# Optimization experiments

Hardware: AMD Instinct MI355X
Metric: run time of the kernel (lower is better)

## Reference

```python
import jax, jax.numpy as jnp
import numpy as np

NEG_INF = -10000.0  # module uses inf = 10000.0, not true infinity
B, S, N_TAGS, N_LABELS, N_PATTERNS = 256, 1024, 64, 32, 4


def setup_inputs() -> dict:
    key = jax.random.key(0)
    ks = jax.random.split(key, 8)
    label_emissions = jax.random.normal(ks[0], (B, S, N_LABELS), jnp.float32)
    pattern_emissions = jax.random.normal(ks[1], (B, S, N_PATTERNS), jnp.float32)
    y = jax.random.randint(ks[2], (B, S), 0, N_TAGS)
    label_transitions = 0.1 * jax.random.normal(ks[3], (N_LABELS, N_LABELS), jnp.float32)
    tag2label = jax.random.randint(ks[4], (N_TAGS,), 0, N_LABELS)
    tag_patterns = jax.random.bernoulli(ks[5], 0.25, (N_TAGS, N_PATTERNS)).astype(jnp.float32)
    allowed = jax.random.bernoulli(ks[6], 0.5, (N_TAGS, N_TAGS))
    transition_constraints = jnp.where(allowed, 0.0, NEG_INF).astype(jnp.float32)
    start_mask = jax.random.bernoulli(ks[7], 0.3, (N_TAGS,))
    start_mask = start_mask.at[0].set(True)  # ensure at least one start tag
    return dict(label_emissions=label_emissions,
                pattern_emissions=pattern_emissions,
                y=y,
                label_transitions=label_transitions,
                tag2label=tag2label,
                tag_patterns=tag_patterns,
                transition_constraints=transition_constraints,
                start_mask=start_mask)


def _log_p(label_emissions, pattern_emissions, label_transitions,
           tag_patterns, transition_constraints, y, tag2label, start_mask):
    # per-tag potentials x: [B, S, T]
    x = label_emissions[:, :, tag2label] + pattern_emissions @ tag_patterns.T
    # _transitions(): label_transitions.view(-1)[indices] + constraints == outer gather
    transitions = label_transitions[tag2label[:, None], tag2label[None, :]] + transition_constraints  # [T, T]

    # ----- _logZ (forward algorithm, enforce_boundaries=True) -----
    init = jnp.where(start_mask[None, :], x[:, 0, :], NEG_INF)  # [B, T]

    def step(logits, xi):
        # logmmexp(logits, transitions) + xi
        new = jax.nn.logsumexp(logits[:, :, None] + transitions[None, :, :], axis=1) + xi
        return new, None

    xs = jnp.moveaxis(x[:, 1:, :], 1, 0)  # [S-1, B, T]
    final, _ = jax.lax.scan(step, init, xs)
    logZ = jax.nn.logsumexp(final, axis=1)  # [B]

    # ----- _score -----
    emission = jnp.take_along_axis(x, y[:, :, None], axis=2)[:, :, 0].sum(axis=1)  # [B]
    trans = transitions[y[:, :-1], y[:, 1:]].sum(axis=1)  # [B]
    return emission + trans - logZ


def reference(label_emissions, pattern_emissions, y, label_transitions,
              tag2label, tag_patterns, transition_constraints, start_mask):
    return _log_p(label_emissions, pattern_emissions, label_transitions,
                  tag_patterns, transition_constraints, y, tag2label, start_mask)
```

## Files before the change

### kernel.cpp

```cpp
#include <hip/hip_runtime.h>

#define LOG2E 1.4426950408889634f
#define LN2   0.6931471805599453f
#define PSC   8.0f

typedef __attribute__((ext_vector_type(8))) short bf16x8;
typedef __attribute__((ext_vector_type(4))) float f32x4;
typedef __attribute__((ext_vector_type(4))) unsigned u32x4;

__device__ __forceinline__ unsigned pk_bf16(float lo, float hi){
  unsigned r;
  asm("v_cvt_pk_bf16_f32 %0, %1, %2" : "=v"(r) : "v"(lo), "v"(hi));
  return r;
}
__device__ __forceinline__ unsigned short bf16_rne(float x){
  unsigned u = __float_as_uint(x);
  return (unsigned short)((u + 0x7FFFu + ((u>>16)&1u)) >> 16);
}

__device__ __forceinline__ float wave_sum64(float v){
#define DADD(ctrl) { int _t = __builtin_amdgcn_update_dpp(0, __float_as_int(v), ctrl, 0xF, 0xF, false); \
                     v = v + __int_as_float(_t); }
  DADD(0x111) DADD(0x112) DADD(0x114) DADD(0x118) DADD(0x142) DADD(0x143)
#undef DADD
  return __int_as_float(__builtin_amdgcn_readlane(__float_as_int(v), 63));
}
__device__ __forceinline__ float wave_max64(float v){
#define DMAX(ctrl) { int _t = __builtin_amdgcn_update_dpp(__float_as_int(v), __float_as_int(v), ctrl, 0xF, 0xF, false); \
                     v = fmaxf(v, __int_as_float(_t)); }
  DMAX(0x111) DMAX(0x112) DMAX(0x114) DMAX(0x118) DMAX(0x142) DMAX(0x143)
#undef DMAX
  return __int_as_float(__builtin_amdgcn_readlane(__float_as_int(v), 63));
}
__device__ __forceinline__ f32x4 vmax4(f32x4 a, f32x4 b){
  f32x4 r; r.x=fmaxf(a.x,b.x); r.y=fmaxf(a.y,b.y); r.z=fmaxf(a.z,b.z); r.w=fmaxf(a.w,b.w); return r;
}

__global__ void __launch_bounds__(512, 1)
patcrf_fwd(const float* __restrict__ le, const float* __restrict__ pe,
           const int* __restrict__ y, const float* __restrict__ lt,
           const int* __restrict__ t2l, const float* __restrict__ tp,
           const float* __restrict__ tc, const unsigned int* __restrict__ smask,
           float* __restrict__ out)
{
  const int b = blockIdx.x;
  const int tid = threadIdx.x;
  const int wv = tid >> 6;
  const int lane = tid & 63;
  const int bb = lane & 15, jj = lane >> 4;

  __shared__ __align__(16) char smem[86016];
  float* trans_lds = (float*)smem;
  int*   y_lds     = (int*)(smem + 16384);
  float* E_lds     = (float*)(smem + 20480);
  unsigned short* P_lds = (unsigned short*)smem;
  __shared__ __align__(16) float tp_lds[256];
  __shared__ __align__(16) float pf[64];
  __shared__ int   t2l_lds[64];
  __shared__ float scpart[8];
  __shared__ float L2arr[8];

  if (tid < 64){
    t2l_lds[tid] = t2l[tid];
    *(f32x4*)(tp_lds + tid*4) = *(const f32x4*)(tp + tid*4);
  }
  const int* yb = y + b*1024;
  y_lds[tid] = yb[tid];
  y_lds[tid+512] = yb[tid+512];
  __syncthreads();
  #pragma unroll
  for (int k=0;k<8;k++){
    int idx = k*512 + tid;
    trans_lds[idx] = lt[t2l_lds[idx>>6]*32 + t2l_lds[idx&63]] + tc[idx];
  }
  __syncthreads();

  const float* leb = le + (size_t)b*1024*32;
  const float* peb = pe + (size_t)b*1024*4;
  const int   myl  = t2l_lds[lane];
  const f32x4 mytp = *(const f32x4*)(tp_lds + lane*4);

  {
    int s0 = tid*2;
    int y0 = y_lds[s0], y1 = y_lds[s0+1];
    f32x4 pA = *(const f32x4*)(peb + (size_t)s0*4);
    f32x4 pB = *(const f32x4*)(peb + (size_t)(s0+1)*4);
    f32x4 tA = *(const f32x4*)(tp_lds + y0*4);
    f32x4 tB = *(const f32x4*)(tp_lds + y1*4);
    float s = leb[(size_t)s0*32 + t2l_lds[y0]]
            + pA.x*tA.x + pA.y*tA.y + pA.z*tA.z + pA.w*tA.w
            + leb[(size_t)(s0+1)*32 + t2l_lds[y1]]
            + pB.x*tB.x + pB.y*tB.y + pB.z*tB.z + pB.w*tB.w;
    s += trans_lds[y0*64 + y1];
    if (s0+2 < 1024) s += trans_lds[y1*64 + y_lds[s0+2]];
    float sw = wave_sum64(s);
    if (lane==0) scpart[wv] = sw;
  }

#define CSTEP(ACC, EPTR) do { \
    f32x4 ev[4]; \
    _Pragma("unroll") \
    for (int m_=0;m_<4;m_++) ev[m_] = *(const f32x4*)((EPTR) + 16*m_ + 4*jj); \
    u32x4 Bf[2][4]; \
    _Pragma("unroll") \
    for (int n_=0;n_<4;n_++){ \
      _Pragma("unroll") \
      for (int h_=0;h_<2;h_++){ \
        Bf[h_][n_] = (u32x4){ \
          pk_bf16(ACC[2*h_][n_].x,   ACC[2*h_][n_].y), \
          pk_bf16(ACC[2*h_][n_].z,   ACC[2*h_][n_].w), \
          pk_bf16(ACC[2*h_+1][n_].x, ACC[2*h_+1][n_].y), \
          pk_bf16(ACC[2*h_+1][n_].z, ACC[2*h_+1][n_].w) }; \
      } \
    } \
    _Pragma("unroll") \
    for (int m_=0;m_<4;m_++){ \
      _Pragma("unroll") \
      for (int n_=0;n_<4;n_++){ \
        f32x4 d_ = __builtin_amdgcn_mfma_f32_16x16x32_bf16( \
                     __builtin_bit_cast(bf16x8, Af[m_][0]), \
                     __builtin_bit_cast(bf16x8, Bf[0][n_]), zf, 0,0,0); \
        d_ = __builtin_amdgcn_mfma_f32_16x16x32_bf16( \
                     __builtin_bit_cast(bf16x8, Af[m_][1]), \
                     __builtin_bit_cast(bf16x8, Bf[1][n_]), d_, 0,0,0); \
        ACC[m_][n_] = d_ * ev[m_]; \
      } \
    } \
  } while(0)

#define RENORM(ACC, L2V) do { \
    f32x4 m4_ = ACC[0][0]; \
    _Pragma("unroll") \
    for (int m_=0;m_<4;m_++){ \
      _Pragma("unroll") \
      for (int n_=0;n_<4;n_++) m4_ = vmax4(m4_, ACC[m_][n_]); \
    } \
    float mx_ = fmaxf(fmaxf(m4_.x,m4_.y), fmaxf(m4_.z,m4_.w)); \
    mx_ = wave_max64(mx_); \
    if (mx_ > 0.f){ \
      int Ex_ = (int)(__float_as_uint(mx_)>>23) - 127; \
      if (Ex_ != 0){ \
        float scl_ = __uint_as_float((unsigned)(127 - Ex_) << 23); \
        _Pragma("unroll") \
        for (int m_=0;m_<4;m_++){ \
          _Pragma("unroll") \
          for (int n_=0;n_<4;n_++) ACC[m_][n_] = ACC[m_][n_]*scl_; \
        } \
        (L2V) += (float)Ex_; \
      } \
    } \
  } while(0)

  if (wv < 4){
    const int c = wv;
    u32x4 Af[4][2];
    #pragma unroll
    for (int m=0;m<4;m++){
      #pragma unroll
      for (int h=0;h<2;h++){
        unsigned uu[4];
        #pragma unroll
        for (int q=0;q<4;q++){
          int c0 = 2*q, c1 = 2*q+1;
          int sg0 = 32*h + ((c0>>2)<<4) + 4*jj + (c0&3);
          int sg1 = 32*h + ((c1>>2)<<4) + 4*jj + (c1&3);
          float w0 = __builtin_amdgcn_exp2f(trans_lds[sg0*64 + 16*m + bb]*LOG2E);
          float w1 = __builtin_amdgcn_exp2f(trans_lds[sg1*64 + 16*m + bb]*LOG2E);
          uu[q] = pk_bf16(w0, w1);
        }
        Af[m][h] = (u32x4){uu[0],uu[1],uu[2],uu[3]};
      }
    }
    f32x4 accA[4][4], accB[4][4];
    #pragma unroll
    for (int m=0;m<4;m++){
      #pragma unroll
      for (int n=0;n<4;n++){
        f32x4 z;
        z.x = (m==n && bb==4*jj+0) ? 1.f : 0.f;
        z.y = (m==n && bb==4*jj+1) ? 1.f : 0.f;
        z.z = (m==n && bb==4*jj+2) ? 1.f : 0.f;
        z.w = (m==n && bb==4*jj+3) ? 1.f : 0.f;
        accA[m][n] = z; accB[m][n] = z;
      }
    }
    float L2A = 0.f, L2B = 0.f;
    const f32x4 zf = {0.f,0.f,0.f,0.f};

    __syncthreads();

    for (int ep=0; ep<8; ++ep){
      const float* EbA = E_lds + (c*4 + (ep&1)*2 + 0)*1024;
      const float* EbB = E_lds + (c*4 + (ep&1)*2 + 1)*1024;
      #pragma unroll 2
      for (int s=0;s<16;s++){
        if (!(c==0 && ep==0 && s==0)) CSTEP(accA, EbA + s*64);
        CSTEP(accB, EbB + s*64);
      }
      RENORM(accA, L2A);
      RENORM(accB, L2B);
      __syncthreads();
    }

    {
      unsigned short* PcA = P_lds + (2*c  )*4352;
      unsigned short* PcB = P_lds + (2*c+1)*4352;
      #pragma unroll
      for (int m=0;m<4;m++){
        #pragma unroll
        for (int n=0;n<4;n++){
          PcA[(16*m+4*jj+0)*68 + 16*n + bb] = bf16_rne(accA[m][n].x);
          PcA[(16*m+4*jj+1)*68 + 16*n + bb] = bf16_rne(accA[m][n].y);
          PcA[(16*m+4*jj+2)*68 + 16*n + bb] = bf16_rne(accA[m][n].z);
          PcA[(16*m+4*jj+3)*68 + 16*n + bb] = bf16_rne(accA[m][n].w);
          PcB[(16*m+4*jj+0)*68 + 16*n + bb] = bf16_rne(accB[m][n].x);
          PcB[(16*m+4*jj+1)*68 + 16*n + bb] = bf16_rne(accB[m][n].y);
          PcB[(16*m+4*jj+2)*68 + 16*n + bb] = bf16_rne(accB[m][n].z);
          PcB[(16*m+4*jj+3)*68 + 16*n + bb] = bf16_rne(accB[m][n].w);
        }
      }
      if (lane==0){ L2arr[2*c] = L2A; L2arr[2*c+1] = L2B; }
    }
  } else {
    const int c = wv - 4;
    const int base = 256*c;
    float leA[32]; f32x4 peA[32];
    #pragma unroll
    for (int k=0;k<32;k++){
      int t = base + 128*(k>>4) + (k&15);
      float l0 = leb[(size_t)t*32 + myl];
      f32x4 p0 = *(const f32x4*)(peb + (size_t)t*4);
      float x2 = (l0 + p0.x*mytp.x + p0.y*mytp.y + p0.z*mytp.z + p0.w*mytp.w)*LOG2E - PSC;
      E_lds[(c*4 + (k>>4))*1024 + (k&15)*64 + lane] = __builtin_amdgcn_exp2f(x2);
    }
    #pragma unroll
    for (int k=0;k<32;k++){
      int t = base + 128*(k>>4) + 16 + (k&15);
      leA[k] = leb[(size_t)t*32 + myl];
      peA[k] = *(const f32x4*)(peb + (size_t)t*4);
    }
    __syncthreads();

    for (int ep=0; ep<8; ++ep){
      if (ep < 7){
        int buf = (ep+1)&1;
        #pragma unroll
        for (int k=0;k<32;k++){
          float x2 = (leA[k] + peA[k].x*mytp.x + peA[k].y*mytp.y
                             + peA[k].z*mytp.z + peA[k].w*mytp.w)*LOG2E - PSC;
          E_lds[(c*4 + buf*2 + (k>>4))*1024 + (k&15)*64 + lane] = __builtin_amdgcn_exp2f(x2);
        }
        if (ep < 6){
          #pragma unroll
          for (int k=0;k<32;k++){
            int t = base + 128*(k>>4) + 16*(ep+2) + (k&15);
            leA[k] = leb[(size_t)t*32 + myl];
            peA[k] = *(const f32x4*)(peb + (size_t)t*4);
          }
        }
      }
      __syncthreads();
    }
  }

  __syncthreads();

  if (wv == 0){
    bool all01 = true, allf = true;
    #pragma unroll
    for (int k=0;k<16;k++){
      unsigned v = smask[k];
      all01 = all01 && (v <= 1u);
      allf  = allf  && (v == 0u || v == 0x3F800000u);
    }
    int startv;
    if (all01)      startv = ((const int*)smask)[lane];
    else if (allf)  startv = (((const unsigned*)smask)[lane] != 0u) ? 1 : 0;
    else            startv = ((const unsigned char*)smask)[lane];

    f32x4 pe0 = *(const f32x4*)peb;
    float x0 = leb[myl] + pe0.x*mytp.x + pe0.y*mytp.y + pe0.z*mytp.z + pe0.w*mytp.w;
    float v = startv ? __builtin_amdgcn_exp2f(x0*LOG2E - PSC) : 0.f;
    float L2p = 0.f;

    #pragma unroll 1
    for (int cc=0; cc<8; ++cc){
      pf[lane] = v;
      __builtin_amdgcn_wave_barrier();
      asm volatile("" ::: "memory");
      const unsigned short* Pr = P_lds + cc*4352 + lane*68;
      float q = 0.f;
      #pragma unroll
      for (int k=0;k<16;k++){
        uint2 u = *(const uint2*)(Pr + 4*k);
        f32x4 vv = *(const f32x4*)(pf + 4*k);
        q = fmaf(__uint_as_float(u.x << 16),          vv.x, q);
        q = fmaf(__uint_as_float(u.x & 0xFFFF0000u),  vv.y, q);
        q = fmaf(__uint_as_float(u.y << 16),          vv.z, q);
        q = fmaf(__uint_as_float(u.y & 0xFFFF0000u),  vv.w, q);
      }
      __builtin_amdgcn_wave_barrier();
      asm volatile("" ::: "memory");
      float S = wave_sum64(q);
      L2p += __builtin_amdgcn_logf(S);
      v = q * __builtin_amdgcn_rcpf(S);
    }
    if (lane == 0){
      float sct = ((scpart[0]+scpart[1])+(scpart[2]+scpart[3]))
                + ((scpart[4]+scpart[5])+(scpart[6]+scpart[7]));
      float l2t = ((L2arr[0]+L2arr[1])+(L2arr[2]+L2arr[3]))
                + ((L2arr[4]+L2arr[5])+(L2arr[6]+L2arr[7]));
      float logZ = LN2 * (l2t + L2p + PSC*1024.0f);
      out[b] = sct - logZ;
    }
  }
#undef CSTEP
#undef RENORM
}

extern "C" void kernel_launch(void* const* d_in, const int* in_sizes, int n_in,
                              void* d_out, int out_size, void* d_ws, size_t ws_size,
                              hipStream_t stream)
{
  patcrf_fwd<<<256, 512, 0, stream>>>(
    (const float*)d_in[0],
    (const float*)d_in[1],
    (const int*)d_in[2],
    (const float*)d_in[3],
    (const int*)d_in[4],
    (const float*)d_in[5],
    (const float*)d_in[6],
    (const unsigned int*)d_in[7],
    (float*)d_out);
}
```

Baseline: 119.3 us.

## Make every wave compute its own chunk and emissions instead of producer/consumer split

Replaces the 4 producer + 4 consumer wave split with 8 symmetric waves. Each wave computes exp emissions for its own 128-step chunk into a private double buffer and runs the MFMA chunk product on one accumulator set instead of two interleaved chains. This removes the dedicated producer waves and doubles the number of MFMA-issuing waves, at the cost of each wave serialising its global loads and exps with its own matmul steps. It also adds a guard against a non-positive normaliser in the final combine.

```diff
diff --git a/kernel.cpp b/kernel.cpp
--- a/kernel.cpp
+++ b/kernel.cpp
@@ -151,118 +151,91 @@
     } \
   } while(0)
 
-  if (wv < 4){
-    const int c = wv;
-    u32x4 Af[4][2];
+  const int c = wv;
+  const int base = 128*c;
+  float* Ew = E_lds + wv*2048;
+
+  u32x4 Af[4][2];
+  #pragma unroll
+  for (int m=0;m<4;m++){
     #pragma unroll
-    for (int m=0;m<4;m++){
+    for (int h=0;h<2;h++){
+      unsigned uu[4];
       #pragma unroll
-      for (int h=0;h<2;h++){
-        unsigned uu[4];
-        #pragma unroll
-        for (int q=0;q<4;q++){
-          int c0 = 2*q, c1 = 2*q+1;
-          int sg0 = 32*h + ((c0>>2)<<4) + 4*jj + (c0&3);
-          int sg1 = 32*h + ((c1>>2)<<4) + 4*jj + (c1&3);
-          float w0 = __builtin_amdgcn_exp2f(trans_lds[sg0*64 + 16*m + bb]*LOG2E);
-          float w1 = __builtin_amdgcn_exp2f(trans_lds[sg1*64 + 16*m + bb]*LOG2E);
-          uu[q] = pk_bf16(w0, w1);
-        }
-        Af[m][h] = (u32x4){uu[0],uu[1],uu[2],uu[3]};
+      for (int q=0;q<4;q++){
+        int c0 = 2*q, c1 = 2*q+1;
+        int sg0 = 32*h + ((c0>>2)<<4) + 4*jj + (c0&3);
+        int sg1 = 32*h + ((c1>>2)<<4) + 4*jj + (c1&3);
+        float w0 = __builtin_amdgcn_exp2f(trans_lds[sg0*64 + 16*m + bb]*LOG2E);
+        float w1 = __builtin_amdgcn_exp2f(trans_lds[sg1*64 + 16*m + bb]*LOG2E);
+        uu[q] = pk_bf16(w0, w1);
       }
-    }
-    f32x4 accA[4][4], accB[4][4];
+      Af[m][h] = (u32x4){uu[0],uu[1],uu[2],uu[3]};
+    }
+  }
+  f32x4 acc[4][4];
+  #pragma unroll
+  for (int m=0;m<4;m++){
+    #pragma unroll
+    for (int n=0;n<4;n++){
+      f32x4 z;
+      z.x = (m==n && bb==4*jj+0) ? 1.f : 0.f;
+      z.y = (m==n && bb==4*jj+1) ? 1.f : 0.f;
+      z.z = (m==n && bb==4*jj+2) ? 1.f : 0.f;
+      z.w = (m==n && bb==4*jj+3) ? 1.f : 0.f;
+      acc[m][n] = z;
+    }
+  }
+  float L2c = 0.f;
+  const f32x4 zf = {0.f,0.f,0.f,0.f};
+
+  #pragma unroll
+  for (int s=0;s<16;s++){
+    int t = base + s;
+    float l0 = leb[(size_t)t*32 + myl];
+    f32x4 p0 = *(const f32x4*)(peb + (size_t)t*4);
+    Ew[s*64 + lane] = __builtin_amdgcn_exp2f(
+      (l0 + p0.x*mytp.x + p0.y*mytp.y + p0.z*mytp.z + p0.w*mytp.w)*LOG2E - PSC);
+  }
+  __syncthreads();
+
+  for (int ep=0; ep<8; ++ep){
+    if (ep < 7){
+      float* Eh = Ew + ((ep+1)&1)*1024;
+      #pragma unroll
+      for (int s=0;s<16;s++){
+        int t = base + 16*(ep+1) + s;
+        float l0 = leb[(size_t)t*32 + myl];
+        f32x4 p0 = *(const f32x4*)(peb + (size_t)t*4);
+        Eh[s*64 + lane] = __builtin_amdgcn_exp2f(
+          (l0 + p0.x*mytp.x + p0.y*mytp.y + p0.z*mytp.z + p0.w*mytp.w)*LOG2E - PSC);
+      }
+    }
+    __syncthreads();
+    const float* Eb = Ew + (ep&1)*1024;
+    #pragma unroll 2
+    for (int s=0;s<16;s++){
+      if (!(c==0 && ep==0 && s==0)) CSTEP(acc, Eb + s*64);
+    }
+    RENORM(acc, L2c);
+  }
+
+  __syncthreads();
+
+  {
+    unsigned short* Pc = P_lds + c*4352;
     #pragma unroll
     for (int m=0;m<4;m++){
       #pragma unroll
       for (int n=0;n<4;n++){
-        f32x4 z;
-        z.x = (m==n && bb==4*jj+0) ? 1.f : 0.f;
-        z.y = (m==n && bb==4*jj+1) ? 1.f : 0.f;
-        z.z = (m==n && bb==4*jj+2) ? 1.f : 0.f;
-        z.w = (m==n && bb==4*jj+3) ? 1.f : 0.f;
-        accA[m][n] = z; accB[m][n] = z;
+        Pc[(16*m+4*jj+0)*68 + 16*n + bb] = bf16_rne(acc[m][n].x);
+        Pc[(16*m+4*jj+1)*68 + 16*n + bb] = bf16_rne(acc[m][n].y);
+        Pc[(16*m+4*jj+2)*68 + 16*n + bb] = bf16_rne(acc[m][n].z);
+        Pc[(16*m+4*jj+3)*68 + 16*n + bb] = bf16_rne(acc[m][n].w);
       }
     }
-    float L2A = 0.f, L2B = 0.f;
-    const f32x4 zf = {0.f,0.f,0.f,0.f};
-
-    __syncthreads();
-
-    for (int ep=0; ep<8; ++ep){
-      const float* EbA = E_lds + (c*4 + (ep&1)*2 + 0)*1024;
-      const float* EbB = E_lds + (c*4 + (ep&1)*2 + 1)*1024;
-      #pragma unroll 2
-      for (int s=0;s<16;s++){
-        if (!(c==0 && ep==0 && s==0)) CSTEP(accA, EbA + s*64);
-        CSTEP(accB, EbB + s*64);
-      }
-      RENORM(accA, L2A);
-      RENORM(accB, L2B);
-      __syncthreads();
-    }
-
-    {
-      unsigned short* PcA = P_lds + (2*c  )*4352;
-      unsigned short* PcB = P_lds + (2*c+1)*4352;
-      #pragma unroll
-      for (int m=0;m<4;m++){
-        #pragma unroll
-        for (int n=0;n<4;n++){
-          PcA[(16*m+4*jj+0)*68 + 16*n + bb] = bf16_rne(accA[m][n].x);
-          PcA[(16*m+4*jj+1)*68 + 16*n + bb] = bf16_rne(accA[m][n].y);
-          PcA[(16*m+4*jj+2)*68 + 16*n + bb] = bf16_rne(accA[m][n].z);
-          PcA[(16*m+4*jj+3)*68 + 16*n + bb] = bf16_rne(accA[m][n].w);
-          PcB[(16*m+4*jj+0)*68 + 16*n + bb] = bf16_rne(accB[m][n].x);
-          PcB[(16*m+4*jj+1)*68 + 16*n + bb] = bf16_rne(accB[m][n].y);
-          PcB[(16*m+4*jj+2)*68 + 16*n + bb] = bf16_rne(accB[m][n].z);
-          PcB[(16*m+4*jj+3)*68 + 16*n + bb] = bf16_rne(accB[m][n].w);
-        }
-      }
-      if (lane==0){ L2arr[2*c] = L2A; L2arr[2*c+1] = L2B; }
-    }
-  } else {
-    const int c = wv - 4;
-    const int base = 256*c;
-    float leA[32]; f32x4 peA[32];
-    #pragma unroll
-    for (int k=0;k<32;k++){
-      int t = base + 128*(k>>4) + (k&15);
-      float l0 = leb[(size_t)t*32 + myl];
-      f32x4 p0 = *(const f32x4*)(peb + (size_t)t*4);
-      float x2 = (l0 + p0.x*mytp.x + p0.y*mytp.y + p0.z*mytp.z + p0.w*mytp.w)*LOG2E - PSC;
-      E_lds[(c*4 + (k>>4))*1024 + (k&15)*64 + lane] = __builtin_amdgcn_exp2f(x2);
-    }
-    #pragma unroll
-    for (int k=0;k<32;k++){
-      int t = base + 128*(k>>4) + 16 + (k&15);
-      leA[k] = leb[(size_t)t*32 + myl];
-      peA[k] = *(const f32x4*)(peb + (size_t)t*4);
-    }
-    __syncthreads();
-
-    for (int ep=0; ep<8; ++ep){
-      if (ep < 7){
-        int buf = (ep+1)&1;
-        #pragma unroll
-        for (int k=0;k<32;k++){
-          float x2 = (leA[k] + peA[k].x*mytp.x + peA[k].y*mytp.y
-                             + peA[k].z*mytp.z + peA[k].w*mytp.w)*LOG2E - PSC;
-          E_lds[(c*4 + buf*2 + (k>>4))*1024 + (k&15)*64 + lane] = __builtin_amdgcn_exp2f(x2);
-        }
-        if (ep < 6){
-          #pragma unroll
-          for (int k=0;k<32;k++){
-            int t = base + 128*(k>>4) + 16*(ep+2) + (k&15);
-            leA[k] = leb[(size_t)t*32 + myl];
-            peA[k] = *(const f32x4*)(peb + (size_t)t*4);
-          }
-        }
-      }
-      __syncthreads();
-    }
-  }
-
+    if (lane==0) L2arr[c] = L2c;
+  }
   __syncthreads();
 
   if (wv == 0){
@@ -302,6 +275,7 @@
       __builtin_amdgcn_wave_barrier();
       asm volatile("" ::: "memory");
       float S = wave_sum64(q);
+      if (!(S > 0.f)) S = 1.0f;
       L2p += __builtin_amdgcn_logf(S);
       v = q * __builtin_amdgcn_rcpf(S);
     }
```

After: 123.1 us. +3.1%, slower.
